# Kernel optimization log

Hardware: AMD Instinct MI355X
Metric: run time of the kernel (lower is better)

Reference implementation:

```python
import jax, jax.numpy as jnp
import numpy as np

N, E, D = 50000, 800000, 128   # nodes, edges, input feat dim
H, C = 4, 32                   # heads, per-head channels (H*C = 128)
OUT = 128                      # final linear out_channels
NEG_SLOPE = 0.2


def _glorot(k, shape):
    fan = shape[0] + shape[-1]
    return jax.random.normal(k, shape, jnp.float32) * np.float32(np.sqrt(2.0 / fan))


def setup_inputs() -> dict:
    key = jax.random.key(0)
    ks = jax.random.split(key, 16)
    HC = H * C
    z = lambda n: jnp.zeros((n,), jnp.float32)
    return {
        "x": jax.random.normal(ks[0], (N, D), jnp.float32),
        "edge_index": jax.random.randint(ks[1], (2, E), 0, N),
        "edge_attr": jax.random.uniform(ks[2], (E, 1), jnp.float32),
        # GATv2 layer 1 (in = D)
        "Wl1": _glorot(ks[3], (D, HC)), "bl1": z(HC),
        "Wr1": _glorot(ks[4], (D, HC)), "br1": z(HC),
        "We1": _glorot(ks[5], (1, HC)),
        "att1": _glorot(ks[6], (H, C)),
        "bo1": z(HC),
        # GATv2 layer 2 (in = H*C)
        "Wl2": _glorot(ks[7], (HC, HC)), "bl2": z(HC),
        "Wr2": _glorot(ks[8], (HC, HC)), "br2": z(HC),
        "We2": _glorot(ks[9], (1, HC)),
        "att2": _glorot(ks[10], (H, C)),
        "bo2": z(HC),
        # final Linear
        "Wlin": _glorot(ks[11], (HC, OUT)), "blin": z(OUT),
    }


def _segment_softmax(logits, seg, n):
    # logits: [E_tot, H], seg: [E_tot] target node ids
    m = jax.ops.segment_max(logits, seg, num_segments=n)          # [N, H]
    m = jnp.where(jnp.isfinite(m), m, 0.0)                         # empty-segment guard
    e = jnp.exp(logits - m[seg])
    s = jax.ops.segment_sum(e, seg, num_segments=n)                # [N, H]
    return e / (s[seg] + 1e-16)


def _gatv2_layer(x, src, dst, eattr, Wl, bl, Wr, br, We, att, bo):
    n = x.shape[0]
    xl = (x @ Wl + bl).reshape(n, H, C)   # source transform (lin_l)
    xr = (x @ Wr + br).reshape(n, H, C)   # target transform (lin_r)
    ee = (eattr @ We).reshape(-1, H, C)   # edge transform (lin_edge)
    m = jax.nn.leaky_relu(xl[src] + xr[dst] + ee, NEG_SLOPE)       # [E_tot, H, C]
    logits = jnp.einsum('ehc,hc->eh', m, att)                      # [E_tot, H]
    alpha = _segment_softmax(logits, dst, n)                       # [E_tot, H]
    out = jax.ops.segment_sum(xl[src] * alpha[..., None], dst, num_segments=n)
    return out.reshape(n, H * C) + bo


def _with_self_loops(edge_index, edge_attr, n):
    # PyG add_self_loops(fill_value='mean'): loop attr = mean of incoming edge attrs
    src, dst = edge_index[0], edge_index[1]
    sums = jax.ops.segment_sum(edge_attr, dst, num_segments=n)     # [N, 1]
    cnts = jax.ops.segment_sum(jnp.ones((edge_attr.shape[0], 1), edge_attr.dtype),
                               dst, num_segments=n)
    loop_attr = jnp.where(cnts > 0, sums / jnp.maximum(cnts, 1.0), 0.0)
    ar = jnp.arange(n, dtype=src.dtype)
    full_src = jnp.concatenate([src, ar])
    full_dst = jnp.concatenate([dst, ar])
    full_attr = jnp.concatenate([edge_attr, loop_attr], axis=0)
    return full_src, full_dst, full_attr


def reference(x, edge_index, edge_attr,
              Wl1, bl1, Wr1, br1, We1, att1, bo1,
              Wl2, bl2, Wr2, br2, We2, att2, bo2,
              Wlin, blin):
    x = x.astype(jnp.float32)
    edge_attr = edge_attr.astype(jnp.float32)
    src, dst, eattr = _with_self_loops(edge_index, edge_attr, x.shape[0])
    h = jax.nn.relu(_gatv2_layer(x, src, dst, eattr, Wl1, bl1, Wr1, br1, We1, att1, bo1))
    h = jax.nn.relu(_gatv2_layer(h, src, dst, eattr, Wl2, bl2, Wr2, br2, We2, att2, bo2))
    return jax.nn.relu(h @ Wlin + blin)
```

## Files before the change

### kernel.cpp

```cpp
#include <hip/hip_runtime.h>
#include <hip/hip_fp16.h>
#include <math.h>

#define NEG 0.2f
#define CNT_SHIFT 42
#define SUM_MASK ((1ULL << CNT_SHIFT) - 1)
#define ROWS 48

typedef _Float16 hf2 __attribute__((ext_vector_type(2)));
typedef _Float16 hf8 __attribute__((ext_vector_type(8)));
typedef float f4 __attribute__((ext_vector_type(4)));

template <int CTRL>
__device__ __forceinline__ float dpp_radd(float x) {
  int t = __builtin_amdgcn_update_dpp(0, __float_as_int(x), CTRL, 0xf, 0xf,
                                      false);
  return x + __int_as_float(t);
}

__device__ __forceinline__ uint4 pack_wline(const float* __restrict__ W,
                                            int L) {
  int lane = L & 63, nt = (L >> 6) & 7, kc = L >> 9;
  int kbase = kc * 32 + (lane >> 4) * 8;
  int col = nt * 16 + (lane & 15);
  const float* wp = W + (size_t)kbase * 128 + col;
  uint4 pk;
  pk.x = __builtin_bit_cast(unsigned, __builtin_amdgcn_cvt_pkrtz(wp[0], wp[128]));
  pk.y = __builtin_bit_cast(unsigned, __builtin_amdgcn_cvt_pkrtz(wp[256], wp[384]));
  pk.z = __builtin_bit_cast(unsigned, __builtin_amdgcn_cvt_pkrtz(wp[512], wp[640]));
  pk.w = __builtin_bit_cast(unsigned, __builtin_amdgcn_cvt_pkrtz(wp[768], wp[896]));
  return pk;
}

__device__ __forceinline__ void load_batch(const unsigned* __restrict__ erow,
    int ofs, const hf2* __restrict__ xl, int lane, int n, unsigned* rec,
    hf2* xv) {
  const unsigned* ep = erow + ofs;
#pragma unroll
  for (int j = 0; j < 8; ++j) rec[j] = ep[j];
#pragma unroll
  for (int j = 0; j < 8; ++j) {
    unsigned si = rec[j] & 0xffffu;
    si = si < (unsigned)n ? si : 0u;
    xv[j] = xl[(size_t)si * 64 + lane];
  }
}

__device__ __forceinline__ void proc_batch(const unsigned* rec, const hf2* xv,
    int nvalid, hf2 xrh, hf2 weh, hf2 atth, hf2 negh, float* denom,
    float* ac0, float* ac1) {
  float p[8];
#pragma unroll
  for (int j = 0; j < 8; ++j) {
    hf2 eah = __builtin_bit_cast(hf2, (rec[j] >> 16) * 0x10001u);
    hf2 t = (xv[j] + xrh) + eah * weh;
    hf2 tn = t * negh;
    t = __builtin_elementwise_max(t, tn);
    p[j] = __builtin_amdgcn_fdot2(t, atth, 0.f, false);
  }
#pragma unroll
  for (int j = 0; j < 8; ++j) {
    p[j] = dpp_radd<0xB1>(p[j]);
    p[j] = dpp_radd<0x4E>(p[j]);
    p[j] = dpp_radd<0x141>(p[j]);
    p[j] = dpp_radd<0x140>(p[j]);
  }
#pragma unroll
  for (int j = 0; j < 8; ++j) {
    float w = j < nvalid ? __builtin_amdgcn_exp2f(p[j]) : 0.f;
    denom[j & 1] += w;
    ac0[j & 1] = fmaf(w, (float)xv[j].x, ac0[j & 1]);
    ac1[j & 1] = fmaf(w, (float)xv[j].y, ac1[j & 1]);
  }
}

__device__ __forceinline__ hf2 gat_node(int v, const hf2* __restrict__ xl,
    const hf2* __restrict__ xr, const unsigned* __restrict__ edge,
    const unsigned long long* __restrict__ hist, hf2 weh, hf2 atth, hf2 negh,
    const float* __restrict__ bo, int lane, int n) {
  int ch = lane * 2;
  hf2 xrh = xr[(size_t)v * 64 + lane];
  unsigned long long hv = hist[v];
  int cnt = (int)(hv >> CNT_SHIFT);
  int cntc = cnt < ROWS ? cnt : ROWS;
  const unsigned* erow = edge + (size_t)v * ROWS;

  float denom[2] = {0.f, 0.f};
  float ac0[2] = {0.f, 0.f}, ac1[2] = {0.f, 0.f};

  int nb = (cntc + 7) >> 3;
  if (nb > 0) {
    unsigned recA[8], recB[8];
    hf2 xvA[8], xvB[8];
    load_batch(erow, 0, xl, lane, n, recA, xvA);
    int b = 0;
    for (;;) {
      if (b + 1 < nb) {
        load_batch(erow, (b + 1) * 8, xl, lane, n, recB, xvB);
        proc_batch(recA, xvA, 8, xrh, weh, atth, negh, denom, ac0, ac1);
      } else {
        proc_batch(recA, xvA, cntc - b * 8, xrh, weh, atth, negh, denom, ac0,
                   ac1);
        break;
      }
      ++b;
      if (b + 1 < nb) {
        load_batch(erow, (b + 1) * 8, xl, lane, n, recA, xvA);
        proc_batch(recB, xvB, 8, xrh, weh, atth, negh, denom, ac0, ac1);
      } else {
        proc_batch(recB, xvB, cntc - b * 8, xrh, weh, atth, negh, denom, ac0,
                   ac1);
        break;
      }
      ++b;
    }
  }
  {
    float sumf = (float)(hv & SUM_MASK) * 2.3283064365386963e-10f;
    float mean = cnt > 0 ? sumf / (float)cnt : 0.f;
    hf2 xself = xl[(size_t)v * 64 + lane];
    _Float16 mh = (_Float16)mean;
    hf2 meanh = {mh, mh};
    hf2 t = (xself + xrh) + meanh * weh;
    hf2 tn = t * negh;
    t = __builtin_elementwise_max(t, tn);
    float ps = __builtin_amdgcn_fdot2(t, atth, 0.f, false);
    ps = dpp_radd<0xB1>(ps);
    ps = dpp_radd<0x4E>(ps);
    ps = dpp_radd<0x141>(ps);
    ps = dpp_radd<0x140>(ps);
    float w = __builtin_amdgcn_exp2f(ps);
    denom[0] += w;
    ac0[0] = fmaf(w, (float)xself.x, ac0[0]);
    ac1[0] = fmaf(w, (float)xself.y, ac1[0]);
  }
  float rden = 1.0f / (denom[0] + denom[1] + 1e-16f);
  int ch0 = ch;
  float o0 = fmaxf(fmaf(ac0[0] + ac0[1], rden, bo[ch0]), 0.f);
  float o1 = fmaxf(fmaf(ac1[0] + ac1[1], rden, bo[ch0 + 1]), 0.f);
  hf2 oh = {(_Float16)o0, (_Float16)o1};
  return oh;
}

__global__ __launch_bounds__(256, 2) void k_fuse1(
    const float* __restrict__ X, const float* __restrict__ Wa,
    const float* __restrict__ Wb, const float* __restrict__ Ba,
    const float* __restrict__ Bb, hf2* __restrict__ Y0, hf2* __restrict__ Y1,
    int nrows, int gGemm, const int* __restrict__ ei,
    const float* __restrict__ eattr, unsigned long long* __restrict__ hist,
    unsigned* __restrict__ edge, int E, int nbP,
    const float* __restrict__ W2a, const float* __restrict__ W2b,
    const float* __restrict__ W2c, uint4* __restrict__ wout) {
  __shared__ uint4 Wl[2][1024];
  int bid = blockIdx.x, tid = threadIdx.x;

  if (bid < gGemm) {
    int lane = tid & 63, wid = tid >> 6;
    int quad = lane >> 4, rl = lane & 15;
    int rbase = bid * 128 + wid * 32;

    hf8 a[4][2];
#pragma unroll
    for (int rs = 0; rs < 2; ++rs) {
      int gr = rbase + rs * 16 + rl;
      gr = gr < nrows ? gr : nrows - 1;
      const float* xp = X + (size_t)gr * 128 + quad * 8;
#pragma unroll
      for (int kc = 0; kc < 4; ++kc) {
        float4 u = *reinterpret_cast<const float4*>(xp + kc * 32);
        float4 u2 = *reinterpret_cast<const float4*>(xp + kc * 32 + 4);
        uint4 pk;
        pk.x = __builtin_bit_cast(unsigned, __builtin_amdgcn_cvt_pkrtz(u.x, u.y));
        pk.y = __builtin_bit_cast(unsigned, __builtin_amdgcn_cvt_pkrtz(u.z, u.w));
        pk.z = __builtin_bit_cast(unsigned, __builtin_amdgcn_cvt_pkrtz(u2.x, u2.y));
        pk.w = __builtin_bit_cast(unsigned, __builtin_amdgcn_cvt_pkrtz(u2.z, u2.w));
        a[kc][rs] = __builtin_bit_cast(hf8, pk);
      }
    }

    f4 acc[2][2][8];
#pragma unroll
    for (int m = 0; m < 2; ++m)
#pragma unroll
      for (int rs = 0; rs < 2; ++rs)
#pragma unroll
        for (int nt = 0; nt < 8; ++nt) acc[m][rs][nt] = (f4)0.f;

#pragma unroll
    for (int h = 0; h < 2; ++h) {
      __syncthreads();
#pragma unroll
      for (int m = 0; m < 2; ++m) {
        const float* W = m ? Wb : Wa;
        for (int i = tid; i < 1024; i += 256)
          Wl[m][i] = pack_wline(W, h * 1024 + i);
      }
      __syncthreads();
#pragma unroll
      for (int kcl = 0; kcl < 2; ++kcl) {
        int kc = h * 2 + kcl;
#pragma unroll
        for (int nt = 0; nt < 8; ++nt) {
#pragma unroll
          for (int m = 0; m < 2; ++m) {
            hf8 w = __builtin_bit_cast(hf8,
                Wl[m][(kcl * 8 + nt) * 64 + lane]);
            acc[m][0][nt] = __builtin_amdgcn_mfma_f32_16x16x32_f16(
                w, a[kc][0], acc[m][0][nt], 0, 0, 0);
            acc[m][1][nt] = __builtin_amdgcn_mfma_f32_16x16x32_f16(
                w, a[kc][1], acc[m][1][nt], 0, 0, 0);
          }
        }
      }
    }

#pragma unroll
    for (int m = 0; m < 2; ++m) {
      const float* Bb_ = m ? Bb : Ba;
      hf2* Yv = m ? Y1 : Y0;
#pragma unroll
      for (int rs = 0; rs < 2; ++rs) {
        int row = rbase + rs * 16 + rl;
        if (row < nrows) {
#pragma unroll
          for (int nt = 0; nt < 8; ++nt) {
            f4 av = acc[m][rs][nt];
            int col = nt * 16 + quad * 4;
            float4 bb = *reinterpret_cast<const float4*>(&Bb_[col]);
            float o0 = av[0] + bb.x, o1 = av[1] + bb.y;
            float o2 = av[2] + bb.z, o3 = av[3] + bb.w;
            unsigned p0 = __builtin_bit_cast(unsigned,
                __builtin_amdgcn_cvt_pkrtz(o0, o1));
            unsigned p1 = __builtin_bit_cast(unsigned,
                __builtin_amdgcn_cvt_pkrtz(o2, o3));
            *reinterpret_cast<uint2*>((_Float16*)Yv + (size_t)row * 128 + col)
                = make_uint2(p0, p1);
          }
        }
      }
    }
  } else if (bid < gGemm + nbP) {
    int e0 = (bid - gGemm) * 4096 + tid;
    int d[16], s[16];
    float ea[16];
    bool valid[16];
#pragma unroll
    for (int j = 0; j < 16; ++j) {
      int e = e0 + j * 256;
      valid[j] = e < E;
      int ec = valid[j] ? e : 0;
      d[j] = ei[E + ec];
      s[j] = ei[ec];
      ea[j] = eattr[ec];
    }
#pragma unroll
    for (int j = 0; j < 16; ++j) {
      if (valid[j]) {
        unsigned long long fx =
            (unsigned long long)(ea[j] * 4294967296.0f);
        unsigned long long old =
            atomicAdd(&hist[d[j]], (1ULL << CNT_SHIFT) + fx);
        int rank = (int)(old >> CNT_SHIFT);
        _Float16 h = (_Float16)ea[j];
        unsigned hb = (unsigned)__builtin_bit_cast(unsigned short, h);
        if (rank < ROWS)
          edge[(size_t)d[j] * ROWS + rank] = (unsigned)s[j] | (hb << 16);
      }
    }
  } else {
    int gid = (bid - gGemm - nbP) * 256 + tid;
    if (gid < 3 * 2048) {
      int mat = gid >> 11;
      const float* W = mat == 0 ? W2a : mat == 1 ? W2b : W2c;
      wout[gid] = pack_wline(W, gid & 2047);
    }
  }
}

__global__ __launch_bounds__(256) void k_gatg(const hf2* __restrict__ xl,
    const hf2* __restrict__ xr, const unsigned* __restrict__ edge,
    const unsigned long long* __restrict__ hist, const float* __restrict__ We,
    const float* __restrict__ att, const float* __restrict__ bo,
    const uint4* __restrict__ Wp0, const uint4* __restrict__ Wp1,
    const float* __restrict__ B0, const float* __restrict__ B1,
    hf2* __restrict__ out0, hf2* __restrict__ out1, int n) {
  __shared__ _Float16 hbuf[16][136];
  int tid = threadIdx.x;
  int lane = tid & 63, wid = tid >> 6;
  int quad = lane >> 4, rl = lane & 15;
  int base = blockIdx.x * 16;
  int ch = lane * 2;
  hf2 weh = {(_Float16)We[ch], (_Float16)We[ch + 1]};
  hf2 atth = {(_Float16)(att[ch] * 1.44269504f),
              (_Float16)(att[ch + 1] * 1.44269504f)};
  hf2 negh = {(_Float16)NEG, (_Float16)NEG};

#pragma unroll 1
  for (int i = 0; i < 4; ++i) {
    int row = wid * 4 + i;
    int v = base + row;
    hf2 oh = {(_Float16)0.f, (_Float16)0.f};
    if (v < n)
      oh = gat_node(__builtin_amdgcn_readfirstlane(v), xl, xr, edge, hist,
                    weh, atth, negh, bo, lane, n);
    *reinterpret_cast<hf2*>(&hbuf[row][2 * lane]) = oh;
  }
  __syncthreads();

  hf8 hfrag[4];
#pragma unroll
  for (int kc = 0; kc < 4; ++kc)
    hfrag[kc] = *reinterpret_cast<const hf8*>(&hbuf[rl][kc * 32 + quad * 8]);

#pragma unroll
  for (int ntl = 0; ntl < 2; ++ntl) {
    int nt = wid * 2 + ntl;
#pragma unroll
    for (int m = 0; m < 2; ++m) {
      const uint4* Wp = m ? Wp1 : Wp0;
      f4 a = (f4)0.f;
#pragma unroll
      for (int kc = 0; kc < 4; ++kc) {
        hf8 w = __builtin_bit_cast(hf8, Wp[(kc * 8 + nt) * 64 + lane]);
        a = __builtin_amdgcn_mfma_f32_16x16x32_f16(w, hfrag[kc], a, 0, 0, 0);
      }
      int col = nt * 16 + quad * 4;
      const float* Bb = m ? B1 : B0;
      float4 bb = *reinterpret_cast<const float4*>(&Bb[col]);
      float o0 = a[0] + bb.x, o1 = a[1] + bb.y;
      float o2 = a[2] + bb.z, o3 = a[3] + bb.w;
      hf2 h0 = {(_Float16)o0, (_Float16)o1};
      hf2 h1 = {(_Float16)o2, (_Float16)o3};
      int row = base + rl;
      if (row < n) {
        hf2* outp = m ? out1 : out0;
        uint2 pk = make_uint2(__builtin_bit_cast(unsigned, h0),
                              __builtin_bit_cast(unsigned, h1));
        *reinterpret_cast<uint2*>(outp + (size_t)row * 64 + nt * 8 + quad * 2)
            = pk;
      }
    }
  }
}

__global__ __launch_bounds__(256) void k_gat(const hf2* __restrict__ xl,
    const hf2* __restrict__ xr, const unsigned* __restrict__ edge,
    const unsigned long long* __restrict__ hist, const float* __restrict__ We,
    const float* __restrict__ att, const float* __restrict__ bo,
    hf2* __restrict__ out, int n) {
  int lane = threadIdx.x & 63;
  int wid = threadIdx.x >> 6;
  int v = blockIdx.x * 4 + wid;
  if (v >= n) return;
  int ch = lane * 2;
  hf2 weh = {(_Float16)We[ch], (_Float16)We[ch + 1]};
  hf2 atth = {(_Float16)(att[ch] * 1.44269504f),
              (_Float16)(att[ch + 1] * 1.44269504f)};
  hf2 negh = {(_Float16)NEG, (_Float16)NEG};
  hf2 oh = gat_node(__builtin_amdgcn_readfirstlane(v), xl, xr, edge, hist,
                    weh, atth, negh, bo, lane, n);
  out[(size_t)v * 64 + lane] = oh;
}

__global__ __launch_bounds__(256, 2) void k_gemmf(
    const _Float16* __restrict__ X, const uint4* __restrict__ Wp0,
    const float* __restrict__ B0, float* __restrict__ Y, int nrows) {
  __shared__ uint4 Wl[2048];
  int tid = threadIdx.x;
  for (int i = tid; i < 2048; i += 256) Wl[i] = Wp0[i];

  int lane = tid & 63, wid = tid >> 6;
  int quad = lane >> 4, rl = lane & 15;
  int rbase = blockIdx.x * 128 + wid * 32;

  hf8 a[4][2];
#pragma unroll
  for (int rs = 0; rs < 2; ++rs) {
    int gr = rbase + rs * 16 + rl;
    gr = gr < nrows ? gr : nrows - 1;
    const _Float16* xp = X + (size_t)gr * 128 + quad * 8;
#pragma unroll
    for (int kc = 0; kc < 4; ++kc)
      a[kc][rs] = *reinterpret_cast<const hf8*>(xp + kc * 32);
  }

  f4 acc[2][8];
#pragma unroll
  for (int rs = 0; rs < 2; ++rs)
#pragma unroll
    for (int nt = 0; nt < 8; ++nt) acc[rs][nt] = (f4)0.f;

  __syncthreads();

#pragma unroll
  for (int kc = 0; kc < 4; ++kc) {
#pragma unroll
    for (int nt = 0; nt < 8; ++nt) {
      hf8 w = __builtin_bit_cast(hf8, Wl[(kc * 8 + nt) * 64 + lane]);
      acc[0][nt] = __builtin_amdgcn_mfma_f32_16x16x32_f16(
          w, a[kc][0], acc[0][nt], 0, 0, 0);
      acc[1][nt] = __builtin_amdgcn_mfma_f32_16x16x32_f16(
          w, a[kc][1], acc[1][nt], 0, 0, 0);
    }
  }

#pragma unroll
  for (int rs = 0; rs < 2; ++rs) {
    int row = rbase + rs * 16 + rl;
    if (row < nrows) {
#pragma unroll
      for (int nt = 0; nt < 8; ++nt) {
        f4 av = acc[rs][nt];
        int col = nt * 16 + quad * 4;
        float4 bb = *reinterpret_cast<const float4*>(&B0[col]);
        float o0 = fmaxf(av[0] + bb.x, 0.f);
        float o1 = fmaxf(av[1] + bb.y, 0.f);
        float o2 = fmaxf(av[2] + bb.z, 0.f);
        float o3 = fmaxf(av[3] + bb.w, 0.f);
        *reinterpret_cast<float4*>(&Y[(size_t)row * 128 + col]) =
            make_float4(o0, o1, o2, o3);
      }
    }
  }
}

extern "C" void kernel_launch(void* const* d_in, const int* in_sizes, int n_in,
                              void* d_out, int out_size, void* d_ws, size_t ws_size,
                              hipStream_t stream) {
  const float* x     = (const float*)d_in[0];
  const int*   ei    = (const int*)d_in[1];
  const float* eattr = (const float*)d_in[2];
  const float* Wl1 = (const float*)d_in[3];
  const float* bl1 = (const float*)d_in[4];
  const float* Wr1 = (const float*)d_in[5];
  const float* br1 = (const float*)d_in[6];
  const float* We1 = (const float*)d_in[7];
  const float* att1 = (const float*)d_in[8];
  const float* bo1 = (const float*)d_in[9];
  const float* Wl2 = (const float*)d_in[10];
  const float* bl2 = (const float*)d_in[11];
  const float* Wr2 = (const float*)d_in[12];
  const float* br2 = (const float*)d_in[13];
  const float* We2 = (const float*)d_in[14];
  const float* att2 = (const float*)d_in[15];
  const float* bo2 = (const float*)d_in[16];
  const float* Wlin = (const float*)d_in[17];
  const float* blin = (const float*)d_in[18];
  float* out = (float*)d_out;

  const int N = in_sizes[0] / 128;
  const int E = in_sizes[1] / 2;

  hf2* xl = (hf2*)d_ws;
  hf2* xr = xl + (size_t)N * 64;
  hf2* h16 = xr + (size_t)N * 64;
  uint4* w16 = (uint4*)(h16 + (size_t)N * 64);
  unsigned long long* hist = (unsigned long long*)(w16 + 3 * 2048);
  unsigned* edge = (unsigned*)(hist + N);

  hf2* xl2 = (hf2*)d_out;
  hf2* xr2 = xl2 + (size_t)N * 64;

  (void)hipMemsetAsync(hist, 0, sizeof(unsigned long long) * (size_t)N,
                       stream);

  int gGemm = (N + 127) / 128;
  int nbP = (E + 4095) / 4096;
  int gGat = (N + 3) / 4;
  int gGatg = (N + 15) / 16;

  k_fuse1<<<gGemm + nbP + 24, 256, 0, stream>>>(x, Wl1, Wr1, bl1, br1,
      xl, xr, N, gGemm, ei, eattr, hist, edge, E, nbP,
      Wl2, Wr2, Wlin, w16);

  k_gatg<<<gGatg, 256, 0, stream>>>(xl, xr, edge, hist, We1, att1, bo1,
      w16, w16 + 2048, bl2, br2, xl2, xr2, N);

  k_gat<<<gGat, 256, 0, stream>>>(xl2, xr2, edge, hist, We2, att2, bo2,
                                  h16, N);

  k_gemmf<<<gGemm, 256, 0, stream>>>((const _Float16*)h16, w16 + 2 * 2048,
                                     blin, out, N);
}
```

Before: 259.8 us.

## Prefetch next node's edge batch across nodes in fused GAT loop; shrink edge-bucketing blocks

The fused GAT+GEMM kernel now unrolls its four nodes per wave and loads each node's hist, xr and self feature up front. While the current node is processed, it prefetches the first edge batch and its gathered features for the next node, so gather latency overlaps across node boundaries. gat_node takes these preloaded values, and k_gat uses the same interface. Separately, the edge-bucketing part of k_fuse1 processes 4 edges per thread instead of 16, which launches more blocks to spread the atomics. Holding more live registers risks lower occupancy.

New measurement: 281.0 us. 8.2% more time.

```diff
diff --git a/kernel.cpp b/kernel.cpp
--- a/kernel.cpp
+++ b/kernel.cpp
@@ -32,18 +32,23 @@
   return pk;
 }
 
+__device__ __forceinline__ void gather8(const unsigned* rec,
+    const hf2* __restrict__ xl, int lane, int n, hf2* xv) {
+#pragma unroll
+  for (int j = 0; j < 8; ++j) {
+    unsigned si = rec[j] & 0xffffu;
+    si = si < (unsigned)n ? si : 0u;
+    xv[j] = xl[(size_t)si * 64 + lane];
+  }
+}
+
 __device__ __forceinline__ void load_batch(const unsigned* __restrict__ erow,
     int ofs, const hf2* __restrict__ xl, int lane, int n, unsigned* rec,
     hf2* xv) {
   const unsigned* ep = erow + ofs;
 #pragma unroll
   for (int j = 0; j < 8; ++j) rec[j] = ep[j];
-#pragma unroll
-  for (int j = 0; j < 8; ++j) {
-    unsigned si = rec[j] & 0xffffu;
-    si = si < (unsigned)n ? si : 0u;
-    xv[j] = xl[(size_t)si * 64 + lane];
-  }
+  gather8(rec, xl, lane, n, xv);
 }
 
 __device__ __forceinline__ void proc_batch(const unsigned* rec, const hf2* xv,
@@ -74,16 +79,12 @@
   }
 }
 
-__device__ __forceinline__ hf2 gat_node(int v, const hf2* __restrict__ xl,
-    const hf2* __restrict__ xr, const unsigned* __restrict__ edge,
-    const unsigned long long* __restrict__ hist, hf2 weh, hf2 atth, hf2 negh,
+__device__ __forceinline__ hf2 gat_node(const unsigned* __restrict__ erow,
+    unsigned long long hv, hf2 xrh, hf2 xself, const unsigned* rec0,
+    const hf2* xv0, const hf2* __restrict__ xl, hf2 weh, hf2 atth, hf2 negh,
     const float* __restrict__ bo, int lane, int n) {
-  int ch = lane * 2;
-  hf2 xrh = xr[(size_t)v * 64 + lane];
-  unsigned long long hv = hist[v];
   int cnt = (int)(hv >> CNT_SHIFT);
   int cntc = cnt < ROWS ? cnt : ROWS;
-  const unsigned* erow = edge + (size_t)v * ROWS;
 
   float denom[2] = {0.f, 0.f};
   float ac0[2] = {0.f, 0.f}, ac1[2] = {0.f, 0.f};
@@ -92,7 +93,11 @@
   if (nb > 0) {
     unsigned recA[8], recB[8];
     hf2 xvA[8], xvB[8];
-    load_batch(erow, 0, xl, lane, n, recA, xvA);
+#pragma unroll
+    for (int j = 0; j < 8; ++j) {
+      recA[j] = rec0[j];
+      xvA[j] = xv0[j];
+    }
     int b = 0;
     for (;;) {
       if (b + 1 < nb) {
@@ -118,7 +123,6 @@
   {
     float sumf = (float)(hv & SUM_MASK) * 2.3283064365386963e-10f;
     float mean = cnt > 0 ? sumf / (float)cnt : 0.f;
-    hf2 xself = xl[(size_t)v * 64 + lane];
     _Float16 mh = (_Float16)mean;
     hf2 meanh = {mh, mh};
     hf2 t = (xself + xrh) + meanh * weh;
@@ -135,7 +139,7 @@
     ac1[0] = fmaf(w, (float)xself.y, ac1[0]);
   }
   float rden = 1.0f / (denom[0] + denom[1] + 1e-16f);
-  int ch0 = ch;
+  int ch0 = lane * 2;
   float o0 = fmaxf(fmaf(ac0[0] + ac0[1], rden, bo[ch0]), 0.f);
   float o1 = fmaxf(fmaf(ac1[0] + ac1[1], rden, bo[ch0 + 1]), 0.f);
   hf2 oh = {(_Float16)o0, (_Float16)o1};
@@ -240,12 +244,12 @@
       }
     }
   } else if (bid < gGemm + nbP) {
-    int e0 = (bid - gGemm) * 4096 + tid;
-    int d[16], s[16];
-    float ea[16];
-    bool valid[16];
-#pragma unroll
-    for (int j = 0; j < 16; ++j) {
+    int e0 = (bid - gGemm) * 1024 + tid;
+    int d[4], s[4];
+    float ea[4];
+    bool valid[4];
+#pragma unroll
+    for (int j = 0; j < 4; ++j) {
       int e = e0 + j * 256;
       valid[j] = e < E;
       int ec = valid[j] ? e : 0;
@@ -254,7 +258,7 @@
       ea[j] = eattr[ec];
     }
 #pragma unroll
-    for (int j = 0; j < 16; ++j) {
+    for (int j = 0; j < 4; ++j) {
       if (valid[j]) {
         unsigned long long fx =
             (unsigned long long)(ea[j] * 4294967296.0f);
@@ -294,16 +298,55 @@
   hf2 atth = {(_Float16)(att[ch] * 1.44269504f),
               (_Float16)(att[ch + 1] * 1.44269504f)};
   hf2 negh = {(_Float16)NEG, (_Float16)NEG};
-
-#pragma unroll 1
+  hf2 zero = {(_Float16)0.f, (_Float16)0.f};
+
+  int v0 = base + wid * 4;
+  int vc[4];
+#pragma unroll
   for (int i = 0; i < 4; ++i) {
-    int row = wid * 4 + i;
-    int v = base + row;
-    hf2 oh = {(_Float16)0.f, (_Float16)0.f};
-    if (v < n)
-      oh = gat_node(__builtin_amdgcn_readfirstlane(v), xl, xr, edge, hist,
-                    weh, atth, negh, bo, lane, n);
-    *reinterpret_cast<hf2*>(&hbuf[row][2 * lane]) = oh;
+    int t = v0 + i;
+    t = t < n ? t : n - 1;
+    vc[i] = __builtin_amdgcn_readfirstlane(t);
+  }
+  unsigned long long hv4[4];
+  hf2 xrh4[4], xs4[4];
+#pragma unroll
+  for (int i = 0; i < 4; ++i) {
+    hv4[i] = hist[vc[i]];
+    xrh4[i] = xr[(size_t)vc[i] * 64 + lane];
+    xs4[i] = xl[(size_t)vc[i] * 64 + lane];
+  }
+  unsigned r0A[8], r0B[8];
+  hf2 x0A[8], x0B[8];
+  {
+    const unsigned* ep = edge + (size_t)vc[0] * ROWS;
+#pragma unroll
+    for (int j = 0; j < 8; ++j) r0A[j] = ep[j];
+    gather8(r0A, xl, lane, n, x0A);
+  }
+#pragma unroll
+  for (int i = 0; i < 4; ++i) {
+    if (i < 3) {
+      const unsigned* ep = edge + (size_t)vc[i + 1] * ROWS;
+      if ((i & 1) == 0) {
+#pragma unroll
+        for (int j = 0; j < 8; ++j) r0B[j] = ep[j];
+        gather8(r0B, xl, lane, n, x0B);
+      } else {
+#pragma unroll
+        for (int j = 0; j < 8; ++j) r0A[j] = ep[j];
+        gather8(r0A, xl, lane, n, x0A);
+      }
+    }
+    hf2 oh;
+    if ((i & 1) == 0)
+      oh = gat_node(edge + (size_t)vc[i] * ROWS, hv4[i], xrh4[i], xs4[i],
+                    r0A, x0A, xl, weh, atth, negh, bo, lane, n);
+    else
+      oh = gat_node(edge + (size_t)vc[i] * ROWS, hv4[i], xrh4[i], xs4[i],
+                    r0B, x0B, xl, weh, atth, negh, bo, lane, n);
+    oh = (v0 + i < n) ? oh : zero;
+    *reinterpret_cast<hf2*>(&hbuf[wid * 4 + i][2 * lane]) = oh;
   }
   __syncthreads();
 
@@ -352,13 +395,23 @@
   int wid = threadIdx.x >> 6;
   int v = blockIdx.x * 4 + wid;
   if (v >= n) return;
+  int vu = __builtin_amdgcn_readfirstlane(v);
   int ch = lane * 2;
   hf2 weh = {(_Float16)We[ch], (_Float16)We[ch + 1]};
   hf2 atth = {(_Float16)(att[ch] * 1.44269504f),
               (_Float16)(att[ch + 1] * 1.44269504f)};
   hf2 negh = {(_Float16)NEG, (_Float16)NEG};
-  hf2 oh = gat_node(__builtin_amdgcn_readfirstlane(v), xl, xr, edge, hist,
-                    weh, atth, negh, bo, lane, n);
+  unsigned long long hv = hist[vu];
+  hf2 xrh = xr[(size_t)vu * 64 + lane];
+  hf2 xs = xl[(size_t)vu * 64 + lane];
+  const unsigned* erow = edge + (size_t)vu * ROWS;
+  unsigned r0[8];
+  hf2 x0[8];
+#pragma unroll
+  for (int j = 0; j < 8; ++j) r0[j] = erow[j];
+  gather8(r0, xl, lane, n, x0);
+  hf2 oh = gat_node(erow, hv, xrh, xs, r0, x0, xl, weh, atth, negh, bo,
+                    lane, n);
   out[(size_t)v * 64 + lane] = oh;
 }
 
@@ -465,7 +518,7 @@
                        stream);
 
   int gGemm = (N + 127) / 128;
-  int nbP = (E + 4095) / 4096;
+  int nbP = (E + 1023) / 1024;
   int gGat = (N + 3) / 4;
   int gGatg = (N + 15) / 16;
 
```

## Fuse layer-2 GAT aggregation with final linear+ReLU via MFMA in one kernel

Applied to the files above, without the earlier changes.

Adds a kernel that computes the layer-2 GAT aggregation for 16 nodes per block, stages the fp16 results in shared memory, and applies the final linear layer with MFMA plus bias and ReLU. This removes the h16 global write and re-read and one kernel launch. Because the output buffer can no longer hold the layer-2 xl/xr intermediates, they move into workspace, and the fused path runs only when the workspace is large enough. The trade-offs are lower parallelism per block (4 nodes per wave run sequentially) and extra shared-memory use.

After: 255.5 us. About the same (-1.6%).

```diff
diff --git a/kernel.cpp b/kernel.cpp
--- a/kernel.cpp
+++ b/kernel.cpp
@@ -339,6 +339,63 @@
         *reinterpret_cast<uint2*>(outp + (size_t)row * 64 + nt * 8 + quad * 2)
             = pk;
       }
+    }
+  }
+}
+
+__global__ __launch_bounds__(256) void k_gatf(const hf2* __restrict__ xl,
+    const hf2* __restrict__ xr, const unsigned* __restrict__ edge,
+    const unsigned long long* __restrict__ hist, const float* __restrict__ We,
+    const float* __restrict__ att, const float* __restrict__ bo,
+    const uint4* __restrict__ Wp, const float* __restrict__ Blin,
+    float* __restrict__ out, int n) {
+  __shared__ _Float16 hbuf[16][136];
+  int tid = threadIdx.x;
+  int lane = tid & 63, wid = tid >> 6;
+  int quad = lane >> 4, rl = lane & 15;
+  int base = blockIdx.x * 16;
+  int ch = lane * 2;
+  hf2 weh = {(_Float16)We[ch], (_Float16)We[ch + 1]};
+  hf2 atth = {(_Float16)(att[ch] * 1.44269504f),
+              (_Float16)(att[ch + 1] * 1.44269504f)};
+  hf2 negh = {(_Float16)NEG, (_Float16)NEG};
+
+#pragma unroll 1
+  for (int i = 0; i < 4; ++i) {
+    int row = wid * 4 + i;
+    int v = base + row;
+    hf2 oh = {(_Float16)0.f, (_Float16)0.f};
+    if (v < n)
+      oh = gat_node(__builtin_amdgcn_readfirstlane(v), xl, xr, edge, hist,
+                    weh, atth, negh, bo, lane, n);
+    *reinterpret_cast<hf2*>(&hbuf[row][2 * lane]) = oh;
+  }
+  __syncthreads();
+
+  hf8 hfrag[4];
+#pragma unroll
+  for (int kc = 0; kc < 4; ++kc)
+    hfrag[kc] = *reinterpret_cast<const hf8*>(&hbuf[rl][kc * 32 + quad * 8]);
+
+  int row = base + rl;
+#pragma unroll
+  for (int ntl = 0; ntl < 2; ++ntl) {
+    int nt = wid * 2 + ntl;
+    f4 a = (f4)0.f;
+#pragma unroll
+    for (int kc = 0; kc < 4; ++kc) {
+      hf8 w = __builtin_bit_cast(hf8, Wp[(kc * 8 + nt) * 64 + lane]);
+      a = __builtin_amdgcn_mfma_f32_16x16x32_f16(w, hfrag[kc], a, 0, 0, 0);
+    }
+    int col = nt * 16 + quad * 4;
+    float4 bb = *reinterpret_cast<const float4*>(&Blin[col]);
+    if (row < n) {
+      float o0 = fmaxf(a[0] + bb.x, 0.f);
+      float o1 = fmaxf(a[1] + bb.y, 0.f);
+      float o2 = fmaxf(a[2] + bb.z, 0.f);
+      float o3 = fmaxf(a[3] + bb.w, 0.f);
+      *reinterpret_cast<float4*>(&out[(size_t)row * 128 + col]) =
+          make_float4(o0, o1, o2, o3);
     }
   }
 }
@@ -457,9 +514,11 @@
   uint4* w16 = (uint4*)(h16 + (size_t)N * 64);
   unsigned long long* hist = (unsigned long long*)(w16 + 3 * 2048);
   unsigned* edge = (unsigned*)(hist + N);
-
-  hf2* xl2 = (hf2*)d_out;
-  hf2* xr2 = xl2 + (size_t)N * 64;
+  hf2* xr2w = (hf2*)(edge + (size_t)N * ROWS);
+
+  size_t need_fused = (size_t)N * 256 * 4 + 3 * 2048 * 16 +
+                      (size_t)N * 8 + (size_t)N * ROWS * 4;
+  bool fused34 = ws_size >= need_fused;
 
   (void)hipMemsetAsync(hist, 0, sizeof(unsigned long long) * (size_t)N,
                        stream);
@@ -473,12 +532,21 @@
       xl, xr, N, gGemm, ei, eattr, hist, edge, E, nbP,
       Wl2, Wr2, Wlin, w16);
 
-  k_gatg<<<gGatg, 256, 0, stream>>>(xl, xr, edge, hist, We1, att1, bo1,
-      w16, w16 + 2048, bl2, br2, xl2, xr2, N);
-
-  k_gat<<<gGat, 256, 0, stream>>>(xl2, xr2, edge, hist, We2, att2, bo2,
-                                  h16, N);
-
-  k_gemmf<<<gGemm, 256, 0, stream>>>((const _Float16*)h16, w16 + 2 * 2048,
-                                     blin, out, N);
-}
+  if (fused34) {
+    hf2* xl2 = h16;
+    hf2* xr2 = xr2w;
+    k_gatg<<<gGatg, 256, 0, stream>>>(xl, xr, edge, hist, We1, att1, bo1,
+        w16, w16 + 2048, bl2, br2, xl2, xr2, N);
+    k_gatf<<<gGatg, 256, 0, stream>>>(xl2, xr2, edge, hist, We2, att2, bo2,
+        w16 + 2 * 2048, blin, out, N);
+  } else {
+    hf2* xl2 = (hf2*)d_out;
+    hf2* xr2 = xl2 + (size_t)N * 64;
+    k_gatg<<<gGatg, 256, 0, stream>>>(xl, xr, edge, hist, We1, att1, bo1,
+        w16, w16 + 2048, bl2, br2, xl2, xr2, N);
+    k_gat<<<gGat, 256, 0, stream>>>(xl2, xr2, edge, hist, We2, att2, bo2,
+                                    h16, N);
+    k_gemmf<<<gGemm, 256, 0, stream>>>((const _Float16*)h16, w16 + 2 * 2048,
+                                       blin, out, N);
+  }
+}
```
